# Optimization experiments

Hardware: AMD Instinct MI355X
Metric: run time of the kernel (lower is better)

## Reference

```python
import jax, jax.numpy as jnp
import numpy as np

H = 512

def _lstm_scan(xs, h0, c0, Wih, Whh, bih, bhh):
    # xs: [T,B,I]; PyTorch gate order i,f,g,o
    def step(carry, x):
        h, c = carry
        gates = x @ Wih.T + bih + h @ Whh.T + bhh  # [B,4H]
        i, f, g, o = jnp.split(gates, 4, axis=-1)
        c = jax.nn.sigmoid(f) * c + jax.nn.sigmoid(i) * jnp.tanh(g)
        h = jax.nn.sigmoid(o) * jnp.tanh(c)
        return (h, c), h
    (h, c), ys = jax.lax.scan(step, (h0, c0), xs)
    return ys, h, c


def setup_inputs() -> dict:
    key = jax.random.key(0)
    ks = jax.random.split(key, 12)
    T, B, I, O = 513, 128, 1, 1
    s = 1.0 / np.sqrt(H)
    u = lambda k, shp: jax.random.uniform(k, shp, jnp.float32, -s, s)
    return {
        "input_seq": jax.random.normal(ks[0], (T, B, I), jnp.float32),
        "h0": jnp.zeros((B, H), jnp.float32),
        "c0": jnp.zeros((B, H), jnp.float32),
        "lstm_Wih": u(ks[1], (4 * H, I)),
        "lstm_Whh": u(ks[2], (4 * H, H)),
        "lstm_bih": u(ks[3], (4 * H,)),
        "lstm_bhh": u(ks[4], (4 * H,)),
        "rnn_Wih": u(ks[5], (H, O)),
        "rnn_Whh": u(ks[6], (H, H)),
        "rnn_bih": u(ks[7], (H,)),
        "rnn_bhh": u(ks[8], (H,)),
        "lin_W": u(ks[9], (O, H)),
        "lin_b": u(ks[10], (O,)),
        "batch_size": 128,
        "pred_length": 32,
    }


def reference(input_seq, h0, c0, lstm_Wih, lstm_Whh, lstm_bih, lstm_bhh,
              rnn_Wih, rnn_Whh, rnn_bih, rnn_bhh, lin_W, lin_b,
              batch_size, pred_length):
    # Encoder LSTM over input_seq[:-1]
    enc_ys, h_enc, _ = _lstm_scan(input_seq[:-1], h0, c0,
                                  lstm_Wih, lstm_Whh, lstm_bih, lstm_bhh)
    enc_bth = jnp.transpose(enc_ys, (1, 0, 2))  # [B,T,H]

    def dec_step(carry, _):
        x, h = carry  # x: [B,1] last prediction, h: [B,H] RNN hidden
        h = jnp.tanh(x @ rnn_Wih.T + rnn_bih + h @ rnn_Whh.T + rnn_bhh)
        # Luong dot-product attention over encoder outputs
        scores = jnp.einsum('bth,bh->bt', enc_bth, h)
        w = jax.nn.softmax(scores, axis=-1)
        ctx = jnp.einsum('bt,bth->bh', w, enc_bth)
        out = jax.nn.relu(ctx @ lin_W.T + lin_b)  # [B,1]
        return (out, h), out

    x0 = input_seq[-1]  # [B,1]
    _, preds = jax.lax.scan(dec_step, (x0, h_enc), None, length=pred_length)
    return preds  # [pred_length, B, 1]
```

## Files before the change

kernel.cpp:

```cpp
#include <hip/hip_runtime.h>
#include <hip/hip_bf16.h>

typedef unsigned short u16;
typedef unsigned int u32;
typedef unsigned long long u64;

#define HD 512
#define BATCH 128
#define TENC 512
#define WPAD 520

typedef float f32x4 __attribute__((ext_vector_type(4)));
typedef short s16x8 __attribute__((ext_vector_type(8)));

__device__ __forceinline__ u16 f2b(float f) {
    u32 u = __float_as_uint(f);
    u32 r = (u + 0x7FFFu + ((u >> 16) & 1u)) >> 16;
    return (u16)r;
}
__device__ __forceinline__ float b2f(u16 h) {
    return __uint_as_float(((u32)h) << 16);
}
__device__ __forceinline__ float sigm(float z) { return 1.0f / (1.0f + __expf(-z)); }
__device__ __forceinline__ float tanh_f(float z) { return 1.0f - 2.0f / (__expf(2.0f * z) + 1.0f); }

__global__ void init_misc(const float* __restrict__ h0, const float* __restrict__ rWhh,
                          u64* __restrict__ hb64, u16* __restrict__ rT) {
    int idx = blockIdx.x * 256 + threadIdx.x;
    if (idx < 65536) {
        int g   = idx >> 13;
        int r   = idx & 8191;
        int p   = r >> 12;
        int ofs = r & 4095;
        int b   = ofs >> 8, jp = ofs & 255;
        u64 v = 0ull;
        if (p == 0) {
            const float* hrow = h0 + (size_t)(g * 16 + b) * HD + jp * 2;
            u32 lo = (u32)f2b(hrow[0]) | ((u32)f2b(hrow[1]) << 16);
            v = (u64)lo;
        }
        hb64[(size_t)(g * 2 + p) * 4096 + b * 256 + jp] = v;
    }
    for (int i = idx; i < 262144; i += 131072) {
        int k = i >> 9, j = i & 511;
        rT[i] = f2b(rWhh[j * 512 + k]);
    }
}

__global__ __launch_bounds__(512, 2) void enc_lstm(
    const float* __restrict__ xseq, const float* __restrict__ c0,
    const float* __restrict__ Wih, const float* __restrict__ Whh,
    const float* __restrict__ bih, const float* __restrict__ bhh,
    u16* __restrict__ enc, u64* __restrict__ hb64) {

    __shared__ u16 hlds[16 * WPAD];
    __shared__ float exg[16 * 132];
    __shared__ float bias_l[128];
    __shared__ float wih_l[128];

    const int tid = threadIdx.x;
    const int g = blockIdx.x & 7;
    const int sl = blockIdx.x >> 3;

    if (tid < 128) {
        int n = (tid >> 5) * 512 + sl * 32 + (tid & 31);
        bias_l[tid] = bih[n] + bhh[n];
        wih_l[tid] = Wih[n];
    }

    const int bT = tid >> 5, jl = tid & 31;
    float c = c0[(g * 16 + bT) * HD + sl * 32 + jl];

    const int lane = tid & 63, wv = tid >> 6;
    const int q = lane >> 4, cl = lane & 15;
    const int R = (wv >> 1) * 32 + (wv & 1) * 16;

    s16x8 bw[16];
    {
        int r = R + cl;
        int grow = (r >> 5) * 512 + sl * 32 + (r & 31);
        const float* wrow = Whh + (size_t)grow * 512;
        #pragma unroll
        for (int ks = 0; ks < 16; ++ks) {
            s16x8 v;
            #pragma unroll
            for (int j = 0; j < 8; ++j)
                v[j] = (short)f2b(wrow[ks * 32 + q * 8 + j]);
            bw[ks] = v;
        }
    }

    u32* hlds32 = (u32*)hlds;
    __syncthreads();

    for (int t = 0; t < TENC; ++t) {
        const u64* src = hb64 + (size_t)(g * 2 + (t & 1)) * 4096;
        const u32 want = (u32)t;
        u64 vv[8];
        #pragma unroll
        for (int i = 0; i < 8; ++i)
            vv[i] = __hip_atomic_load(src + tid + i * 512, __ATOMIC_RELAXED,
                                      __HIP_MEMORY_SCOPE_AGENT);
        float xv = xseq[t * BATCH + g * 16 + bT];
        for (;;) {
            bool ok = true;
            #pragma unroll
            for (int i = 0; i < 8; ++i) {
                if ((u32)(vv[i] >> 32) != want) {
                    ok = false;
                    vv[i] = __hip_atomic_load(src + tid + i * 512, __ATOMIC_RELAXED,
                                              __HIP_MEMORY_SCOPE_AGENT);
                }
            }
            if (ok) break;
        }
        #pragma unroll
        for (int i = 0; i < 8; ++i) {
            int idx = tid + i * 512;
            int b = idx >> 8, w = idx & 255;
            hlds32[b * 260 + w] = (u32)vv[i];
        }
        __syncthreads();

        f32x4 acc = {0.f, 0.f, 0.f, 0.f};
        #pragma unroll
        for (int ks = 0; ks < 16; ++ks) {
            s16x8 av = *(const s16x8*)&hlds[cl * WPAD + ks * 32 + q * 8];
            acc = __builtin_amdgcn_mfma_f32_16x16x32_bf16(av, bw[ks], acc, 0, 0, 0);
        }
        #pragma unroll
        for (int r4 = 0; r4 < 4; ++r4)
            exg[(q * 4 + r4) * 132 + R + cl] = acc[r4];
        __syncthreads();

        const float* exb = &exg[bT * 132];
        float gi = exb[jl]      + xv * wih_l[jl]      + bias_l[jl];
        float gf = exb[32 + jl] + xv * wih_l[32 + jl] + bias_l[32 + jl];
        float gg = exb[64 + jl] + xv * wih_l[64 + jl] + bias_l[64 + jl];
        float go = exb[96 + jl] + xv * wih_l[96 + jl] + bias_l[96 + jl];
        c = sigm(gf) * c + sigm(gi) * tanh_f(gg);
        float hv = sigm(go) * tanh_f(c);
        u16 h16 = f2b(hv);
        int jgl = sl * 32 + jl;

        u32 me = (u32)h16;
        u32 up = (u32)__shfl_down((int)me, 1, 64);
        if ((jl & 1) == 0) {
            u64 word = (u64)(me | (up << 16)) | ((u64)(u32)(t + 1) << 32);
            __hip_atomic_store(hb64 + (size_t)(g * 2 + ((t + 1) & 1)) * 4096
                                    + bT * 256 + (jgl >> 1),
                               word, __ATOMIC_RELAXED, __HIP_MEMORY_SCOPE_AGENT);
        }
        enc[((size_t)t * BATCH + g * 16 + bT) * HD + jgl] = h16;
    }
}

__global__ __launch_bounds__(512, 2) void dec_all(
    const float* __restrict__ xlast, const u16* __restrict__ enc,
    const u16* __restrict__ rT, const float* __restrict__ rWih,
    const float* __restrict__ rbih, const float* __restrict__ rbhh,
    const float* __restrict__ linW, const float* __restrict__ linb,
    float* __restrict__ dout) {

    __shared__ float hp[512];
    __shared__ float ctxl[8 * 512];
    __shared__ float red[512];
    __shared__ float mw[8], lw[8];
    __shared__ float xsh;

    const int tid = threadIdx.x;
    const int b = blockIdx.x;
    const int wv = tid >> 6, lane = tid & 63;

    hp[tid] = b2f(enc[(size_t)511 * BATCH * HD + b * HD + tid]);
    float x = xlast[b];
    const float bia = rbih[tid] + rbhh[tid];
    const float wih = rWih[tid];
    const float lwt = linW[tid];
    const float lb = linb[0];
    const uint4* rT4 = (const uint4*)rT;
    const u16* ebase = enc + (size_t)b * HD + lane * 8;
    __syncthreads();

    for (int s = 0; s < 32; ++s) {
        uint4 buf[4];
        #pragma unroll
        for (int i = 0; i < 4; ++i)
            buf[i] = *(const uint4*)(ebase + (size_t)(i * 8 + wv) * 65536);

        float pa[8] = {0, 0, 0, 0, 0, 0, 0, 0};
        const uint4* base = rT4 + (size_t)(wv * 64) * 64 + lane;
        #pragma unroll 4
        for (int kk = 0; kk < 64; ++kk) {
            float hk = hp[wv * 64 + kk];
            uint4 w = base[kk * 64];
            pa[0] = fmaf(hk, b2f((u16)(w.x & 0xFFFF)), pa[0]);
            pa[1] = fmaf(hk, b2f((u16)(w.x >> 16)),    pa[1]);
            pa[2] = fmaf(hk, b2f((u16)(w.y & 0xFFFF)), pa[2]);
            pa[3] = fmaf(hk, b2f((u16)(w.y >> 16)),    pa[3]);
            pa[4] = fmaf(hk, b2f((u16)(w.z & 0xFFFF)), pa[4]);
            pa[5] = fmaf(hk, b2f((u16)(w.z >> 16)),    pa[5]);
            pa[6] = fmaf(hk, b2f((u16)(w.w & 0xFFFF)), pa[6]);
            pa[7] = fmaf(hk, b2f((u16)(w.w >> 16)),    pa[7]);
        }
        #pragma unroll
        for (int i = 0; i < 8; ++i) ctxl[wv * 512 + lane * 8 + i] = pa[i];
        __syncthreads();

        float a = bia + x * wih;
        #pragma unroll
        for (int i = 0; i < 8; ++i) a += ctxl[i * 512 + tid];
        float hv = tanh_f(a);
        red[tid] = hv;
        __syncthreads();

        float h8[8];
        #pragma unroll
        for (int i = 0; i < 8; ++i) h8[i] = red[lane * 8 + i];
        float m = -1e30f, l = 0.f;
        float acc[8] = {0, 0, 0, 0, 0, 0, 0, 0};
        for (int blk = 0; blk < 16; ++blk) {
            uint4 nxt[4];
            if (blk < 15) {
                #pragma unroll
                for (int i = 0; i < 4; ++i)
                    nxt[i] = *(const uint4*)(ebase +
                               (size_t)((blk + 1) * 32 + i * 8 + wv) * 65536);
            }
            #pragma unroll
            for (int i = 0; i < 4; ++i) {
                uint4 ev = buf[i];
                float e[8];
                e[0] = b2f((u16)(ev.x & 0xFFFF)); e[1] = b2f((u16)(ev.x >> 16));
                e[2] = b2f((u16)(ev.y & 0xFFFF)); e[3] = b2f((u16)(ev.y >> 16));
                e[4] = b2f((u16)(ev.z & 0xFFFF)); e[5] = b2f((u16)(ev.z >> 16));
                e[6] = b2f((u16)(ev.w & 0xFFFF)); e[7] = b2f((u16)(ev.w >> 16));
                float sp = 0.f;
                #pragma unroll
                for (int j = 0; j < 8; ++j) sp = fmaf(e[j], h8[j], sp);
                #pragma unroll
                for (int mk = 1; mk < 64; mk <<= 1) sp += __shfl_xor(sp, mk, 64);
                if (sp > m) {
                    float sc = __expf(m - sp);
                    l *= sc;
                    #pragma unroll
                    for (int j = 0; j < 8; ++j) acc[j] *= sc;
                    m = sp;
                }
                float p = __expf(sp - m);
                l += p;
                #pragma unroll
                for (int j = 0; j < 8; ++j) acc[j] = fmaf(p, e[j], acc[j]);
            }
            #pragma unroll
            for (int i = 0; i < 4; ++i) buf[i] = nxt[i];
        }
        if (lane == 0) { mw[wv] = m; lw[wv] = l; }
        #pragma unroll
        for (int i = 0; i < 8; ++i) ctxl[wv * HD + lane * 8 + i] = acc[i];
        __syncthreads();

        float M = mw[0];
        #pragma unroll
        for (int i = 1; i < 8; ++i) M = fmaxf(M, mw[i]);
        float L = 0.f, aw[8];
        #pragma unroll
        for (int i = 0; i < 8; ++i) { aw[i] = __expf(mw[i] - M); L += aw[i] * lw[i]; }
        float cj = 0.f;
        #pragma unroll
        for (int i = 0; i < 8; ++i) cj = fmaf(aw[i], ctxl[i * HD + tid], cj);
        float r = cj * lwt;
        #pragma unroll
        for (int mk = 1; mk < 64; mk <<= 1) r += __shfl_xor(r, mk, 64);
        if (lane == 0) red[wv] = r;
        __syncthreads();
        if (tid == 0) {
            float o = (red[0] + red[1] + red[2] + red[3] +
                       red[4] + red[5] + red[6] + red[7]) / L + lb;
            o = fmaxf(o, 0.f);
            dout[s * BATCH + b] = o;
            xsh = o;
        }
        __syncthreads();
        x = xsh;
        hp[tid] = hv;
        __syncthreads();
    }
}

extern "C" void kernel_launch(void* const* d_in, const int* in_sizes, int n_in,
                              void* d_out, int out_size, void* d_ws, size_t ws_size,
                              hipStream_t stream) {
    const float* xseq = (const float*)d_in[0];
    const float* h0   = (const float*)d_in[1];
    const float* c0   = (const float*)d_in[2];
    const float* Wih  = (const float*)d_in[3];
    const float* Whh  = (const float*)d_in[4];
    const float* bih  = (const float*)d_in[5];
    const float* bhh  = (const float*)d_in[6];
    const float* rWih = (const float*)d_in[7];
    const float* rWhh = (const float*)d_in[8];
    const float* rbih = (const float*)d_in[9];
    const float* rbhh = (const float*)d_in[10];
    const float* linW = (const float*)d_in[11];
    const float* linb = (const float*)d_in[12];
    float* dout = (float*)d_out;

    char* ws = (char*)d_ws;
    u16* enc  = (u16*)ws;
    u16* rT   = (u16*)(ws + 67108864);
    u64* hb64 = (u64*)(ws + 67108864 + 524288);

    init_misc<<<512, 256, 0, stream>>>(h0, rWhh, hb64, rT);
    enc_lstm<<<128, 512, 0, stream>>>(xseq, c0, Wih, Whh, bih, bhh, enc, hb64);
    dec_all<<<128, 512, 0, stream>>>(xseq + 512 * BATCH, enc, rT, rWih,
                                     rbih, rbhh, linW, linb, dout);
}
```

Baseline: 2.567 ms.

## Batch attention score reductions and split MFMA accumulators for ILP

The decoder attention loop now processes 8 timesteps per iteration. It does 8 independent cross-lane shuffle reductions together and one online-softmax rescale per batch instead of per timestep, and it doubles the prefetch depth to 8 uint4 loads. The launch bound drops to 1 block per SM so the kernel has enough registers for this. In the encoder, the MFMA chain is split into two independent accumulators to break the dependency, and the handoff store pointers are precomputed. The trade-off is higher register pressure and lower occupancy in the decoder.

Measured after the change: 2.372 ms, median of 2. -7.6%, faster.

```diff
diff --git a/kernel.cpp b/kernel.cpp
--- a/kernel.cpp
+++ b/kernel.cpp
@@ -93,6 +93,10 @@
     u32* hlds32 = (u32*)hlds;
     __syncthreads();
 
+    const int jgl = sl * 32 + jl;
+    u64* dpl0 = hb64 + (size_t)(g * 2) * 4096 + bT * 256 + (jgl >> 1);
+    u64* dpl1 = dpl0 + 4096;
+
     for (int t = 0; t < TENC; ++t) {
         const u64* src = hb64 + (size_t)(g * 2 + (t & 1)) * 4096;
         const u32 want = (u32)t;
@@ -117,17 +121,19 @@
         #pragma unroll
         for (int i = 0; i < 8; ++i) {
             int idx = tid + i * 512;
-            int b = idx >> 8, w = idx & 255;
-            hlds32[b * 260 + w] = (u32)vv[i];
-        }
-        __syncthreads();
-
-        f32x4 acc = {0.f, 0.f, 0.f, 0.f};
-        #pragma unroll
-        for (int ks = 0; ks < 16; ++ks) {
-            s16x8 av = *(const s16x8*)&hlds[cl * WPAD + ks * 32 + q * 8];
-            acc = __builtin_amdgcn_mfma_f32_16x16x32_bf16(av, bw[ks], acc, 0, 0, 0);
-        }
+            hlds32[(idx >> 8) * 260 + (idx & 255)] = (u32)vv[i];
+        }
+        __syncthreads();
+
+        f32x4 acc0 = {0.f, 0.f, 0.f, 0.f}, acc1 = {0.f, 0.f, 0.f, 0.f};
+        #pragma unroll
+        for (int ks = 0; ks < 16; ks += 2) {
+            s16x8 av0 = *(const s16x8*)&hlds[cl * WPAD + ks * 32 + q * 8];
+            s16x8 av1 = *(const s16x8*)&hlds[cl * WPAD + (ks + 1) * 32 + q * 8];
+            acc0 = __builtin_amdgcn_mfma_f32_16x16x32_bf16(av0, bw[ks], acc0, 0, 0, 0);
+            acc1 = __builtin_amdgcn_mfma_f32_16x16x32_bf16(av1, bw[ks + 1], acc1, 0, 0, 0);
+        }
+        f32x4 acc = acc0 + acc1;
         #pragma unroll
         for (int r4 = 0; r4 < 4; ++r4)
             exg[(q * 4 + r4) * 132 + R + cl] = acc[r4];
@@ -141,21 +147,19 @@
         c = sigm(gf) * c + sigm(gi) * tanh_f(gg);
         float hv = sigm(go) * tanh_f(c);
         u16 h16 = f2b(hv);
-        int jgl = sl * 32 + jl;
 
         u32 me = (u32)h16;
         u32 up = (u32)__shfl_down((int)me, 1, 64);
         if ((jl & 1) == 0) {
             u64 word = (u64)(me | (up << 16)) | ((u64)(u32)(t + 1) << 32);
-            __hip_atomic_store(hb64 + (size_t)(g * 2 + ((t + 1) & 1)) * 4096
-                                    + bT * 256 + (jgl >> 1),
-                               word, __ATOMIC_RELAXED, __HIP_MEMORY_SCOPE_AGENT);
+            __hip_atomic_store(((t + 1) & 1) ? dpl1 : dpl0, word,
+                               __ATOMIC_RELAXED, __HIP_MEMORY_SCOPE_AGENT);
         }
         enc[((size_t)t * BATCH + g * 16 + bT) * HD + jgl] = h16;
     }
 }
 
-__global__ __launch_bounds__(512, 2) void dec_all(
+__global__ __launch_bounds__(512, 1) void dec_all(
     const float* __restrict__ xlast, const u16* __restrict__ enc,
     const u16* __restrict__ rT, const float* __restrict__ rWih,
     const float* __restrict__ rbih, const float* __restrict__ rbhh,
@@ -183,11 +187,6 @@
     __syncthreads();
 
     for (int s = 0; s < 32; ++s) {
-        uint4 buf[4];
-        #pragma unroll
-        for (int i = 0; i < 4; ++i)
-            buf[i] = *(const uint4*)(ebase + (size_t)(i * 8 + wv) * 65536);
-
         float pa[8] = {0, 0, 0, 0, 0, 0, 0, 0};
         const uint4* base = rT4 + (size_t)(wv * 64) * 64 + lane;
         #pragma unroll 4
@@ -219,41 +218,59 @@
         for (int i = 0; i < 8; ++i) h8[i] = red[lane * 8 + i];
         float m = -1e30f, l = 0.f;
         float acc[8] = {0, 0, 0, 0, 0, 0, 0, 0};
-        for (int blk = 0; blk < 16; ++blk) {
-            uint4 nxt[4];
-            if (blk < 15) {
-                #pragma unroll
-                for (int i = 0; i < 4; ++i)
+
+        uint4 buf[8];
+        #pragma unroll
+        for (int i = 0; i < 8; ++i)
+            buf[i] = *(const uint4*)(ebase + (size_t)(i * 8 + wv) * 65536);
+
+        for (int it = 0; it < 8; ++it) {
+            uint4 nxt[8];
+            if (it < 7) {
+                #pragma unroll
+                for (int i = 0; i < 8; ++i)
                     nxt[i] = *(const uint4*)(ebase +
-                               (size_t)((blk + 1) * 32 + i * 8 + wv) * 65536);
-            }
-            #pragma unroll
-            for (int i = 0; i < 4; ++i) {
+                               (size_t)((it + 1) * 64 + i * 8 + wv) * 65536);
+            }
+            float e[8][8], sp[8];
+            #pragma unroll
+            for (int i = 0; i < 8; ++i) {
                 uint4 ev = buf[i];
-                float e[8];
-                e[0] = b2f((u16)(ev.x & 0xFFFF)); e[1] = b2f((u16)(ev.x >> 16));
-                e[2] = b2f((u16)(ev.y & 0xFFFF)); e[3] = b2f((u16)(ev.y >> 16));
-                e[4] = b2f((u16)(ev.z & 0xFFFF)); e[5] = b2f((u16)(ev.z >> 16));
-                e[6] = b2f((u16)(ev.w & 0xFFFF)); e[7] = b2f((u16)(ev.w >> 16));
-                float sp = 0.f;
-                #pragma unroll
-                for (int j = 0; j < 8; ++j) sp = fmaf(e[j], h8[j], sp);
-                #pragma unroll
-                for (int mk = 1; mk < 64; mk <<= 1) sp += __shfl_xor(sp, mk, 64);
-                if (sp > m) {
-                    float sc = __expf(m - sp);
-                    l *= sc;
-                    #pragma unroll
-                    for (int j = 0; j < 8; ++j) acc[j] *= sc;
-                    m = sp;
-                }
-                float p = __expf(sp - m);
+                e[i][0] = b2f((u16)(ev.x & 0xFFFF)); e[i][1] = b2f((u16)(ev.x >> 16));
+                e[i][2] = b2f((u16)(ev.y & 0xFFFF)); e[i][3] = b2f((u16)(ev.y >> 16));
+                e[i][4] = b2f((u16)(ev.z & 0xFFFF)); e[i][5] = b2f((u16)(ev.z >> 16));
+                e[i][6] = b2f((u16)(ev.w & 0xFFFF)); e[i][7] = b2f((u16)(ev.w >> 16));
+                float sd = 0.f;
+                #pragma unroll
+                for (int j = 0; j < 8; ++j) sd = fmaf(e[i][j], h8[j], sd);
+                sp[i] = sd;
+            }
+            #pragma unroll
+            for (int mk = 1; mk < 64; mk <<= 1) {
+                #pragma unroll
+                for (int i = 0; i < 8; ++i) sp[i] += __shfl_xor(sp[i], mk, 64);
+            }
+            float pm = sp[0];
+            #pragma unroll
+            for (int i = 1; i < 8; ++i) pm = fmaxf(pm, sp[i]);
+            if (pm > m) {
+                float sc = __expf(m - pm);
+                l *= sc;
+                #pragma unroll
+                for (int j = 0; j < 8; ++j) acc[j] *= sc;
+                m = pm;
+            }
+            #pragma unroll
+            for (int i = 0; i < 8; ++i) {
+                float p = __expf(sp[i] - m);
                 l += p;
                 #pragma unroll
-                for (int j = 0; j < 8; ++j) acc[j] = fmaf(p, e[j], acc[j]);
-            }
-            #pragma unroll
-            for (int i = 0; i < 4; ++i) buf[i] = nxt[i];
+                for (int j = 0; j < 8; ++j) acc[j] = fmaf(p, e[i][j], acc[j]);
+            }
+            if (it < 7) {
+                #pragma unroll
+                for (int i = 0; i < 8; ++i) buf[i] = nxt[i];
+            }
         }
         if (lane == 0) { mw[wv] = m; lw[wv] = l; }
         #pragma unroll
```
